# Kernel optimization log

Measured on AMD Instinct MI355X. Metric: run time of the kernel, lower is better.

## Reference

```python
import jax, jax.numpy as jnp
import numpy as np

EPS = 1e-8  # matches F.cosine_similarity default eps
N_CLASSES = 10


def _mlp(x, W1, b1, W2, b2):
    # Embedding MLP: Linear -> ReLU -> Linear (dims=[64,128,64])
    h = jax.nn.relu(x @ W1 + b1)
    return h @ W2 + b2


def setup_inputs() -> dict:
    key = jax.random.key(0)
    ks = jax.random.split(key, 5)
    d_in, d_hid, d_out = 64, 128, 64
    B_test, B_train = 8192, 16384
    X = jax.random.normal(ks[0], (B_test, d_in), dtype=jnp.float32)
    x_train = jax.random.normal(ks[1], (B_train, d_in), dtype=jnp.float32)
    y_train = jax.random.randint(ks[2], (B_train,), 0, N_CLASSES)
    W1 = jax.random.normal(ks[3], (d_in, d_hid), dtype=jnp.float32) * (1.0 / np.sqrt(d_in))
    b1 = jnp.zeros((d_hid,), dtype=jnp.float32)
    W2 = jax.random.normal(ks[4], (d_hid, d_out), dtype=jnp.float32) * (1.0 / np.sqrt(d_hid))
    b2 = jnp.zeros((d_out,), dtype=jnp.float32)
    return {"X": X, "x_train": x_train, "y_train": y_train,
            "W1": W1, "b1": b1, "W2": W2, "b2": b2}


def reference(X, x_train, y_train, W1, b1, W2, b2):
    test_embd = _mlp(X, W1, b1, W2, b2)          # [B_test, d]
    train_embd = _mlp(x_train, W1, b1, W2, b2)   # [B_train, d]
    # Cosine similarity between every (test, train) pair, vectorized.
    # F.cosine_similarity: dot / max(||a||*||b||, eps)
    dots = test_embd @ train_embd.T                       # [B_test, B_train]
    tn = jnp.linalg.norm(test_embd, axis=1, keepdims=True)   # [B_test, 1]
    sn = jnp.linalg.norm(train_embd, axis=1, keepdims=True)  # [B_train, 1]
    sims = dots / jnp.maximum(tn * sn.T, EPS)
    proba = jax.nn.softmax(sims, axis=1)                  # attention over train set
    one_hot = jax.nn.one_hot(y_train, N_CLASSES, dtype=proba.dtype)  # [B_train, C]
    # Weighted one-hot vote: replaces the per-row Python loop with a matmul.
    preds = proba @ one_hot                               # [B_test, C]
    return preds
```

## Files before the change

kernel.cpp:

```cpp
#include <hip/hip_runtime.h>
#include <hip/hip_bf16.h>


typedef __attribute__((ext_vector_type(8))) short short8;
typedef __attribute__((ext_vector_type(4))) float floatx4;
typedef unsigned short u16;

__device__ __forceinline__ u16 f2bf(float f) {
    unsigned u = __float_as_uint(f);
    u += 0x7fffu + ((u >> 16) & 1u);
    return (u16)(u >> 16);
}

__global__ __launch_bounds__(256) void k_prep(
    const float* __restrict__ W1, const float* __restrict__ W2,
    const int* __restrict__ y, u16* __restrict__ W1f,
    u16* __restrict__ W2f, u16* __restrict__ Vf)
{
    int tid = blockIdx.x * 256 + threadIdx.x;
    if (tid < 8192) {
        int k = tid >> 7, n = tid & 127;
        int fid = (n >> 4) * 2 + (k >> 5);
        int l   = ((k >> 3) & 3) * 16 + (n & 15);
        W1f[fid * 512 + l * 8 + (k & 7)] = f2bf(W1[k * 128 + n]);
        int k2 = tid >> 6, n2 = tid & 63;
        int fid2 = (n2 >> 4) * 4 + (k2 >> 5);
        int l2   = ((k2 >> 3) & 3) * 16 + (n2 & 15);
        W2f[fid2 * 512 + l2 * 8 + (k2 & 7)] = f2bf(W2[k2 * 64 + n2]);
    }
    if (tid < 262144) {
        int j = tid >> 4, c = tid & 15;
        float v = (c < 10) ? ((y[j] == c) ? 1.f : 0.f) : ((c == 10) ? 1.f : 0.f);
        int fid = j >> 5;
        int l   = ((j >> 3) & 3) * 16 + c;
        Vf[fid * 512 + l * 8 + (j & 7)] = f2bf(v);
    }
}

#define HSTR 136

__global__ __launch_bounds__(256) void k_embed(
    const float* __restrict__ X, const float* __restrict__ Xtr,
    const u16* __restrict__ W1f, const float* __restrict__ b1,
    const u16* __restrict__ W2f, const float* __restrict__ b2,
    u16* __restrict__ Etf, u16* __restrict__ Etrf)
{
    __shared__ __align__(16) u16 Hbuf[4][16][HSTR];
    const int w = threadIdx.x >> 6, lane = threadIdx.x & 63;
    const int m = lane & 15, g = lane >> 4;
    const int strip = blockIdx.x * 4 + w;
    const int row0  = strip * 16;
    const bool isTest = (row0 < 8192);
    const float* src = isTest ? (X + (size_t)row0 * 64)
                              : (Xtr + (size_t)(row0 - 8192) * 64);
    const floatx4 fz = {0.f, 0.f, 0.f, 0.f};

    const float* prow = src + m * 64;
    short8 a0, a1;
    {
        floatx4 x0 = *(const floatx4*)(prow + g * 8);
        floatx4 x1 = *(const floatx4*)(prow + g * 8 + 4);
        floatx4 x2 = *(const floatx4*)(prow + 32 + g * 8);
        floatx4 x3 = *(const floatx4*)(prow + 32 + g * 8 + 4);
        #pragma unroll
        for (int j = 0; j < 4; j++) { a0[j] = (short)f2bf(x0[j]); a0[4 + j] = (short)f2bf(x1[j]); }
        #pragma unroll
        for (int j = 0; j < 4; j++) { a1[j] = (short)f2bf(x2[j]); a1[4 + j] = (short)f2bf(x3[j]); }
    }

    #pragma unroll
    for (int nt = 0; nt < 8; nt++) {
        short8 bw0 = *(const short8*)(W1f + (nt * 2 + 0) * 512 + lane * 8);
        short8 bw1 = *(const short8*)(W1f + (nt * 2 + 1) * 512 + lane * 8);
        floatx4 acc = __builtin_amdgcn_mfma_f32_16x16x32_bf16(a0, bw0, fz, 0, 0, 0);
        acc = __builtin_amdgcn_mfma_f32_16x16x32_bf16(a1, bw1, acc, 0, 0, 0);
        float bias = b1[nt * 16 + m];
        #pragma unroll
        for (int r = 0; r < 4; r++) {
            float h = acc[r] + bias;
            h = h > 0.f ? h : 0.f;
            Hbuf[w][g * 4 + r][nt * 16 + m] = f2bf(h);
        }
    }

    short8 ha[4];
    #pragma unroll
    for (int kt = 0; kt < 4; kt++)
        ha[kt] = *(const short8*)(&Hbuf[w][m][kt * 32 + g * 8]);

    float ef[4][4];
    #pragma unroll
    for (int nt = 0; nt < 4; nt++) {
        floatx4 acc = fz;
        #pragma unroll
        for (int kt = 0; kt < 4; kt++) {
            short8 bw = *(const short8*)(W2f + (nt * 4 + kt) * 512 + lane * 8);
            acc = __builtin_amdgcn_mfma_f32_16x16x32_bf16(ha[kt], bw, acc, 0, 0, 0);
        }
        float bias = b2[nt * 16 + m];
        #pragma unroll
        for (int r = 0; r < 4; r++) ef[nt][r] = acc[r] + bias;
    }

    float rn[4];
    #pragma unroll
    for (int r = 0; r < 4; r++) {
        float ss = 0.f;
        #pragma unroll
        for (int nt = 0; nt < 4; nt++) ss += ef[nt][r] * ef[nt][r];
        ss += __shfl_xor(ss, 1);
        ss += __shfl_xor(ss, 2);
        ss += __shfl_xor(ss, 4);
        ss += __shfl_xor(ss, 8);
        rn[r] = rsqrtf(fmaxf(ss, 1e-30f));
    }

    u16* dst = isTest ? Etf : Etrf;
    const int stile = (isTest ? row0 : row0 - 8192) >> 4;
    #pragma unroll
    for (int nt = 0; nt < 4; nt++) {
        int col = nt * 16 + m;
        int kt = col >> 5, gg = (col >> 3) & 3, jj = col & 7;
        #pragma unroll
        for (int r = 0; r < 4; r++) {
            int rloc = g * 4 + r;
            dst[(stile * 2 + kt) * 512 + (gg * 16 + rloc) * 8 + jj] =
                f2bf(ef[nt][r] * rn[r]);
        }
    }
}

#define TS 8
#define PSTR 40

__global__ __launch_bounds__(256, 4) void k_main(
    const u16* __restrict__ Etf, const u16* __restrict__ Etrf,
    const u16* __restrict__ Vf, float* __restrict__ acc)
{
    __shared__ __align__(16) u16 Pbuf[4][64][PSTR];
    __shared__ float Obuf[4][64][16];
    const int w = threadIdx.x >> 6, lane = threadIdx.x & 63;
    const int m = lane & 15, g = lane >> 4;
    const int bx = blockIdx.x, by = blockIdx.y;
    const floatx4 fz = {0.f, 0.f, 0.f, 0.f};

    short8 a[4][2];
    #pragma unroll
    for (int ms = 0; ms < 4; ms++) {
        int stile = bx * 4 + ms;
        a[ms][0] = *(const short8*)(Etf + (stile * 2 + 0) * 512 + lane * 8);
        a[ms][1] = *(const short8*)(Etf + (stile * 2 + 1) * 512 + lane * 8);
    }

    floatx4 o[4] = {fz, fz, fz, fz};
    const int wstart = by * 2048 + w * 512;

    for (int tg = 0; tg < 16; tg++) {
        const int tb32 = wstart + tg * 32;
        short8 vfrag = *(const short8*)(Vf + (tb32 >> 5) * 512 + lane * 8);

        #pragma unroll
        for (int half = 0; half < 2; half++) {
            const int tb = tb32 + half * 16;
            const int f = tb >> 4;
            short8 b0 = *(const short8*)(Etrf + (f * 2 + 0) * 512 + lane * 8);
            short8 b1 = *(const short8*)(Etrf + (f * 2 + 1) * 512 + lane * 8);
            #pragma unroll
            for (int ms = 0; ms < 4; ms++) {
                floatx4 s = __builtin_amdgcn_mfma_f32_16x16x32_bf16(a[ms][0], b0, fz, 0, 0, 0);
                s = __builtin_amdgcn_mfma_f32_16x16x32_bf16(a[ms][1], b1, s, 0, 0, 0);
                #pragma unroll
                for (int r = 0; r < 4; r++) {
                    float p = __expf(s[r]);
                    Pbuf[w][ms * 16 + g * 4 + r][half * 16 + m] = f2bf(p);
                }
            }
        }
        #pragma unroll
        for (int ms = 0; ms < 4; ms++) {
            short8 pa = *(const short8*)(&Pbuf[w][ms * 16 + m][g * 8]);
            o[ms] = __builtin_amdgcn_mfma_f32_16x16x32_bf16(pa, vfrag, o[ms], 0, 0, 0);
        }
    }

    #pragma unroll
    for (int ms = 0; ms < 4; ms++)
        #pragma unroll
        for (int r = 0; r < 4; r++)
            Obuf[w][ms * 16 + g * 4 + r][m] = o[ms][r];
    __syncthreads();
    for (int i = threadIdx.x; i < 1024; i += 256) {
        int mm = i >> 4, c = i & 15;
        float s = Obuf[0][mm][c] + Obuf[1][mm][c] + Obuf[2][mm][c] + Obuf[3][mm][c];
        atomicAdd(&acc[(bx * 64 + mm) * 16 + c], s);
    }
}

__global__ __launch_bounds__(256) void k_final(
    const float* __restrict__ acc, float* __restrict__ out)
{
    int row = blockIdx.x * 256 + threadIdx.x;
    if (row < 8192) {
        float inv = 1.0f / acc[row * 16 + 10];
        #pragma unroll
        for (int c = 0; c < 10; c++)
            out[row * 10 + c] = acc[row * 16 + c] * inv;
    }
}

extern "C" void kernel_launch(void* const* d_in, const int* in_sizes, int n_in,
                              void* d_out, int out_size, void* d_ws, size_t ws_size,
                              hipStream_t stream)
{
    const float* X   = (const float*)d_in[0];
    const float* Xtr = (const float*)d_in[1];
    const int*   y   = (const int*)d_in[2];
    const float* W1  = (const float*)d_in[3];
    const float* b1  = (const float*)d_in[4];
    const float* W2  = (const float*)d_in[5];
    const float* b2  = (const float*)d_in[6];
    float* out = (float*)d_out;

    char* ws = (char*)d_ws;
    float* acc = (float*)ws;
    u16* Etf  = (u16*)(ws + 524288);
    u16* Etrf = (u16*)(ws + 524288 + 1048576);
    u16* W1f  = (u16*)(ws + 524288 + 1048576 + 2097152);
    u16* W2f  = W1f + 8192;
    u16* Vf   = W2f + 8192;

    hipMemsetAsync(acc, 0, 8192 * 16 * sizeof(float), stream);
    k_prep<<<1024, 256, 0, stream>>>(W1, W2, y, W1f, W2f, Vf);
    k_embed<<<384, 256, 0, stream>>>(X, Xtr, W1f, b1, W2f, b2, Etf, Etrf);
    k_main<<<dim3(128, TS), 256, 0, stream>>>(Etf, Etrf, Vf, acc);
    k_final<<<32, 256, 0, stream>>>(acc, out);
}
```

Baseline: 113.6 us.

## Transpose score MFMA for packed P stores, use exp2, replace atomics with partial buffers

Swaps the MFMA operand roles so each lane holds four consecutive train columns of a test row. Those four exp values are packed into bf16 pairs with perm and written as two 32-bit LDS stores instead of eight 16-bit stores. The log2(e) factor is folded into the test-embedding normalization so the kernel can call the hardware exp2 directly. The memset and global atomicAdd are replaced by per-slice partial buffers that k_final reduces with vector loads, at the cost of a larger workspace and extra reads in the final kernel.

```diff
diff --git a/kernel.cpp b/kernel.cpp
--- a/kernel.cpp
+++ b/kernel.cpp
@@ -5,6 +5,9 @@
 typedef __attribute__((ext_vector_type(8))) short short8;
 typedef __attribute__((ext_vector_type(4))) float floatx4;
 typedef unsigned short u16;
+typedef unsigned int u32;
+
+#define LOG2E 1.4426950408889634f
 
 __device__ __forceinline__ u16 f2bf(float f) {
     unsigned u = __float_as_uint(f);
@@ -102,6 +105,7 @@
         for (int r = 0; r < 4; r++) ef[nt][r] = acc[r] + bias;
     }
 
+    const float sc = isTest ? LOG2E : 1.0f;
     float rn[4];
     #pragma unroll
     for (int r = 0; r < 4; r++) {
@@ -112,7 +116,7 @@
         ss += __shfl_xor(ss, 2);
         ss += __shfl_xor(ss, 4);
         ss += __shfl_xor(ss, 8);
-        rn[r] = rsqrtf(fmaxf(ss, 1e-30f));
+        rn[r] = rsqrtf(fmaxf(ss, 1e-30f)) * sc;
     }
 
     u16* dst = isTest ? Etf : Etrf;
@@ -135,7 +139,7 @@
 
 __global__ __launch_bounds__(256, 4) void k_main(
     const u16* __restrict__ Etf, const u16* __restrict__ Etrf,
-    const u16* __restrict__ Vf, float* __restrict__ acc)
+    const u16* __restrict__ Vf, float* __restrict__ accp)
 {
     __shared__ __align__(16) u16 Pbuf[4][64][PSTR];
     __shared__ float Obuf[4][64][16];
@@ -144,12 +148,12 @@
     const int bx = blockIdx.x, by = blockIdx.y;
     const floatx4 fz = {0.f, 0.f, 0.f, 0.f};
 
-    short8 a[4][2];
-    #pragma unroll
-    for (int ms = 0; ms < 4; ms++) {
-        int stile = bx * 4 + ms;
-        a[ms][0] = *(const short8*)(Etf + (stile * 2 + 0) * 512 + lane * 8);
-        a[ms][1] = *(const short8*)(Etf + (stile * 2 + 1) * 512 + lane * 8);
+    short8 b[4][2];
+    #pragma unroll
+    for (int ns = 0; ns < 4; ns++) {
+        int stile = bx * 4 + ns;
+        b[ns][0] = *(const short8*)(Etf + (stile * 2 + 0) * 512 + lane * 8);
+        b[ns][1] = *(const short8*)(Etf + (stile * 2 + 1) * 512 + lane * 8);
     }
 
     floatx4 o[4] = {fz, fz, fz, fz};
@@ -161,19 +165,21 @@
 
         #pragma unroll
         for (int half = 0; half < 2; half++) {
-            const int tb = tb32 + half * 16;
-            const int f = tb >> 4;
-            short8 b0 = *(const short8*)(Etrf + (f * 2 + 0) * 512 + lane * 8);
-            short8 b1 = *(const short8*)(Etrf + (f * 2 + 1) * 512 + lane * 8);
+            const int f = (tb32 >> 4) + half;
+            short8 a0 = *(const short8*)(Etrf + (f * 2 + 0) * 512 + lane * 8);
+            short8 a1 = *(const short8*)(Etrf + (f * 2 + 1) * 512 + lane * 8);
             #pragma unroll
-            for (int ms = 0; ms < 4; ms++) {
-                floatx4 s = __builtin_amdgcn_mfma_f32_16x16x32_bf16(a[ms][0], b0, fz, 0, 0, 0);
-                s = __builtin_amdgcn_mfma_f32_16x16x32_bf16(a[ms][1], b1, s, 0, 0, 0);
-                #pragma unroll
-                for (int r = 0; r < 4; r++) {
-                    float p = __expf(s[r]);
-                    Pbuf[w][ms * 16 + g * 4 + r][half * 16 + m] = f2bf(p);
-                }
+            for (int ns = 0; ns < 4; ns++) {
+                floatx4 s = __builtin_amdgcn_mfma_f32_16x16x32_bf16(a0, b[ns][0], fz, 0, 0, 0);
+                s = __builtin_amdgcn_mfma_f32_16x16x32_bf16(a1, b[ns][1], s, 0, 0, 0);
+                u32 p0 = __float_as_uint(__builtin_amdgcn_exp2f(s[0]));
+                u32 p1 = __float_as_uint(__builtin_amdgcn_exp2f(s[1]));
+                u32 p2 = __float_as_uint(__builtin_amdgcn_exp2f(s[2]));
+                u32 p3 = __float_as_uint(__builtin_amdgcn_exp2f(s[3]));
+                u32 pk0 = __builtin_amdgcn_perm(p1, p0, 0x07060302u);
+                u32 pk1 = __builtin_amdgcn_perm(p3, p2, 0x07060302u);
+                u32* dst = (u32*)&Pbuf[w][ns * 16 + m][half * 16 + g * 4];
+                dst[0] = pk0; dst[1] = pk1;
             }
         }
         #pragma unroll
@@ -192,19 +198,32 @@
     for (int i = threadIdx.x; i < 1024; i += 256) {
         int mm = i >> 4, c = i & 15;
         float s = Obuf[0][mm][c] + Obuf[1][mm][c] + Obuf[2][mm][c] + Obuf[3][mm][c];
-        atomicAdd(&acc[(bx * 64 + mm) * 16 + c], s);
+        accp[((size_t)by * 8192 + bx * 64 + mm) * 16 + c] = s;
     }
 }
 
 __global__ __launch_bounds__(256) void k_final(
-    const float* __restrict__ acc, float* __restrict__ out)
+    const float* __restrict__ accp, float* __restrict__ out)
 {
     int row = blockIdx.x * 256 + threadIdx.x;
     if (row < 8192) {
-        float inv = 1.0f / acc[row * 16 + 10];
-        #pragma unroll
-        for (int c = 0; c < 10; c++)
-            out[row * 10 + c] = acc[row * 16 + c] * inv;
+        floatx4 s0 = {0.f,0.f,0.f,0.f}, s1 = s0, s2 = s0;
+        #pragma unroll
+        for (int p = 0; p < TS; p++) {
+            const floatx4* src = (const floatx4*)(accp + ((size_t)p * 8192 + row) * 16);
+            s0 += src[0]; s1 += src[1]; s2 += src[2];
+        }
+        float inv = 1.0f / s2[2];
+        out[row * 10 + 0] = s0[0] * inv;
+        out[row * 10 + 1] = s0[1] * inv;
+        out[row * 10 + 2] = s0[2] * inv;
+        out[row * 10 + 3] = s0[3] * inv;
+        out[row * 10 + 4] = s1[0] * inv;
+        out[row * 10 + 5] = s1[1] * inv;
+        out[row * 10 + 6] = s1[2] * inv;
+        out[row * 10 + 7] = s1[3] * inv;
+        out[row * 10 + 8] = s2[0] * inv;
+        out[row * 10 + 9] = s2[1] * inv;
     }
 }
 
@@ -222,16 +241,15 @@
     float* out = (float*)d_out;
 
     char* ws = (char*)d_ws;
-    float* acc = (float*)ws;
-    u16* Etf  = (u16*)(ws + 524288);
-    u16* Etrf = (u16*)(ws + 524288 + 1048576);
-    u16* W1f  = (u16*)(ws + 524288 + 1048576 + 2097152);
+    float* accp = (float*)ws;
+    u16* Etf  = (u16*)(ws + 4194304);
+    u16* Etrf = (u16*)(ws + 4194304 + 1048576);
+    u16* W1f  = (u16*)(ws + 4194304 + 1048576 + 2097152);
     u16* W2f  = W1f + 8192;
     u16* Vf   = W2f + 8192;
 
-    hipMemsetAsync(acc, 0, 8192 * 16 * sizeof(float), stream);
     k_prep<<<1024, 256, 0, stream>>>(W1, W2, y, W1f, W2f, Vf);
     k_embed<<<384, 256, 0, stream>>>(X, Xtr, W1f, b1, W2f, b2, Etf, Etrf);
-    k_main<<<dim3(128, TS), 256, 0, stream>>>(Etf, Etrf, Vf, acc);
-    k_final<<<32, 256, 0, stream>>>(acc, out);
-}
+    k_main<<<dim3(128, TS), 256, 0, stream>>>(Etf, Etrf, Vf, accp);
+    k_final<<<32, 256, 0, stream>>>(accp, out);
+}
```

After: 103.0 us. 1.1x faster.
